# Optimization experiments

Hardware: AMD Instinct MI355X
Metric: run time of the kernel (lower is better)

The kernel has to match this reference:

```python
import jax, jax.numpy as jnp
import numpy as np
import math

B_, M_, T_, E_ = 4, 4, 128, 512
S_ = M_ * T_
H_ = 2048
NE, NS, TOPK, NHEAD = 8, 2, 2, 4
P_, GRUH, AK, AV = 128, 128, 64, 64


def _ln(x, s, b, eps=1e-5):
    mu = x.mean(-1, keepdims=True)
    var = x.var(-1, keepdims=True)
    return (x - mu) / jnp.sqrt(var + eps) * s + b


def _gru(x, Wih, bih, Whh, bhh):
    # x: [N, T, D] -> [N, T, GRUH]; torch nn.GRU cell equations
    Hh = Whh.shape[1]
    def step(h, xt):
        gi = xt @ Wih.T + bih
        gh = h @ Whh.T + bhh
        ir, iz, inn = jnp.split(gi, 3, axis=-1)
        hr, hz, hn = jnp.split(gh, 3, axis=-1)
        r = jax.nn.sigmoid(ir + hr)
        z = jax.nn.sigmoid(iz + hz)
        n = jnp.tanh(inn + r * hn)
        h = (1.0 - z) * n + z * h
        return h, h
    h0 = jnp.zeros((x.shape[0], Hh), x.dtype)
    _, hs = jax.lax.scan(step, h0, jnp.swapaxes(x, 0, 1))
    return jnp.swapaxes(hs, 0, 1)


def _router_logits(x4, rU, rR, rS, Wtp, btp, Wq, bq, Wk, bk, Wv, bv,
                   gWih, gbih, gWhh, gbhh, mW1, mb1, mW2, mb2):
    B, M, T, E = x4.shape
    proc = jax.nn.relu(x4 @ Wtp + btp)                  # [B,M,T,P]
    q = proc @ Wq + bq                                   # [B,M,T,AK]
    Rp = jnp.transpose(rR, (0, 3, 1, 2))                 # [B,T,M,M]
    Sp = jnp.transpose(rS, (0, 3, 1, 2))
    others = np.array([[j for j in range(M) if j != m] for m in range(M)])  # [M,M-1]
    mi = np.arange(M)[:, None]
    feat = jnp.stack([Rp[:, :, mi, others], Sp[:, :, mi, others]], axis=-1)  # [B,T,M,M-1,2]
    keys = feat @ Wk + bk                                # [B,T,M,M-1,AK]
    vals = feat @ Wv + bv                                # [B,T,M,M-1,AV]
    sc = jnp.einsum('bmtk,btmok->bmto', q, keys) / math.sqrt(AK)
    ctx = jnp.einsum('bmto,btmov->bmtv', jax.nn.softmax(sc, -1), vals)  # [B,M,T,AV]
    gin = jnp.concatenate([rU[..., None], ctx], -1).reshape(B * M, T, 1 + AV)
    hs = _gru(gin, gWih, gbih, gWhh, gbhh).reshape(B, M, T, GRUH)
    comb = jnp.concatenate([proc, hs], -1)               # [B,M,T,P+GRUH]
    return jax.nn.relu(comb @ mW1 + mb1) @ mW2 + mb2     # [B,M,T,NE]


def _forward(x, rU, rR, rS, M, T, Wtp, btp, Wq, bq, Wk, bk, Wv, bv,
             gWih, gbih, gWhh, gbhh, mW1, mb1, mW2, mb2,
             sWq, sbq, sWk, sbk, sWv, sbv, sWo, sbo, sln1s, sln1b,
             sW1, sb1, sW2, sb2, sln2s, sln2b, fW1, fb1, fW2, fb2):
    B, S, E = x.shape
    x4 = x.reshape(B, M, T, E)
    logits = _router_logits(x4, rU, rR, rS, Wtp, btp, Wq, bq, Wk, bk, Wv, bv,
                            gWih, gbih, gWhh, gbhh, mW1, mb1, mW2, mb2)
    NT = B * S
    lf = logits.reshape(NT, NE)
    probs = jax.nn.softmax(lf, -1)
    vals, idx = jax.lax.top_k(lf, TOPK)
    tw = jax.nn.softmax(vals, -1)                        # renormalized top-k weights
    tok = x.reshape(NT, E)
    out = jnp.zeros((NT, E), x.dtype)
    hd = E // NHEAD
    for e in range(NE):
        w = jnp.sum(jnp.where(idx == e, tw, 0.0), -1)    # [NT] per-token weight for expert e
        if e < NS:
            # synergy expert: self-attention restricted to tokens routed here.
            # Sort routed tokens to the front (fixed capacity NT) and mask keys.
            valid = w > 0
            order = jnp.argsort(jnp.where(valid, 0, 1), stable=True)
            xg, vg = tok[order], valid[order]
            qh = (xg @ sWq[e] + sbq[e]).reshape(NT, NHEAD, hd)
            kh = (xg @ sWk[e] + sbk[e]).reshape(NT, NHEAD, hd)
            vh = (xg @ sWv[e] + sbv[e]).reshape(NT, NHEAD, hd)
            sc = jnp.einsum('nhd,mhd->hnm', qh, kh) / math.sqrt(hd)
            sc = jnp.where(vg[None, None, :], sc, -1e9)
            ao = jnp.einsum('hnm,mhd->nhd', jax.nn.softmax(sc, -1), vh).reshape(NT, E)
            ao = ao @ sWo[e] + sbo[e]
            h1 = _ln(xg + ao, sln1s[e], sln1b[e])
            ff = jax.nn.relu(h1 @ sW1[e] + sb1[e]) @ sW2[e] + sb2[e]
            y = _ln(h1 + ff, sln2s[e], sln2b[e])
            out = out.at[order].add(y * w[order][:, None])
        else:
            # FFN expert is pointwise -> dense compute weighted by w (w==0 elsewhere)
            f = e - NS
            y = jax.nn.relu(tok @ fW1[f] + fb1[f]) @ fW2[f] + fb2[f]
            out = out + y * w[:, None]
    return (out.reshape(B, S, E), probs.reshape(B, M, T, NE),
            idx.reshape(B, M, T, TOPK))


def setup_inputs() -> dict:
    key = jax.random.key(0)
    ks = iter(jax.random.split(key, 64))
    def rn(shape, s=0.02):
        return jax.random.normal(next(ks), shape, dtype=jnp.float32) * s
    Cm = (P_ + GRUH) // 2
    return {
        'x': jax.random.normal(next(ks), (B_, S_, E_), dtype=jnp.float32),
        'rU': jax.random.uniform(next(ks), (B_, M_, T_), dtype=jnp.float32),
        'rR': jax.random.uniform(next(ks), (B_, M_, M_, T_), dtype=jnp.float32),
        'rS': jax.random.uniform(next(ks), (B_, M_, M_, T_), dtype=jnp.float32),
        'M': M_, 'T': T_,
        'Wtp': rn((E_, P_)), 'btp': jnp.zeros((P_,)),
        'Wq': rn((P_, AK)), 'bq': jnp.zeros((AK,)),
        'Wk': rn((2, AK)), 'bk': jnp.zeros((AK,)),
        'Wv': rn((2, AV)), 'bv': jnp.zeros((AV,)),
        'gWih': rn((3 * GRUH, 1 + AV)), 'gbih': jnp.zeros((3 * GRUH,)),
        'gWhh': rn((3 * GRUH, GRUH)), 'gbhh': jnp.zeros((3 * GRUH,)),
        'mW1': rn((P_ + GRUH, Cm)), 'mb1': jnp.zeros((Cm,)),
        'mW2': rn((Cm, NE)), 'mb2': jnp.zeros((NE,)),
        'sWq': rn((NS, E_, E_)), 'sbq': jnp.zeros((NS, E_)),
        'sWk': rn((NS, E_, E_)), 'sbk': jnp.zeros((NS, E_)),
        'sWv': rn((NS, E_, E_)), 'sbv': jnp.zeros((NS, E_)),
        'sWo': rn((NS, E_, E_)), 'sbo': jnp.zeros((NS, E_)),
        'sln1s': jnp.ones((NS, E_)), 'sln1b': jnp.zeros((NS, E_)),
        'sW1': rn((NS, E_, H_)), 'sb1': jnp.zeros((NS, H_)),
        'sW2': rn((NS, H_, E_)), 'sb2': jnp.zeros((NS, E_)),
        'sln2s': jnp.ones((NS, E_)), 'sln2b': jnp.zeros((NS, E_)),
        'fW1': rn((NE - NS, E_, H_)), 'fb1': jnp.zeros((NE - NS, H_)),
        'fW2': rn((NE - NS, H_, E_)), 'fb2': jnp.zeros((NE - NS, E_)),
    }


def reference(x, rU, rR, rS, M, T, Wtp, btp, Wq, bq, Wk, bk, Wv, bv,
              gWih, gbih, gWhh, gbhh, mW1, mb1, mW2, mb2,
              sWq, sbq, sWk, sbk, sWv, sbv, sWo, sbo, sln1s, sln1b,
              sW1, sb1, sW2, sb2, sln2s, sln2b, fW1, fb1, fW2, fb2):
    return _forward(x, rU, rR, rS, M, T, Wtp, btp, Wq, bq, Wk, bk, Wv, bv,
                    gWih, gbih, gWhh, gbhh, mW1, mb1, mW2, mb2,
                    sWq, sbq, sWk, sbk, sWv, sbv, sWo, sbo, sln1s, sln1b,
                    sW1, sb1, sW2, sb2, sln2s, sln2b, fW1, fb1, fW2, fb2)
```

## Files before the change

### kernel.cpp

```cpp
#include <hip/hip_runtime.h>
#include <math.h>

#define Bc 4
#define Mc 4
#define Tc 128
#define Ec 512
#define Hc 2048
#define NEc 8
#define NSc 2
#define NHEADc 4
#define Pc 128
#define GRUHc 128
#define AKc 64
#define AVc 64
#define NTc 2048
#define HDc 128

typedef __bf16 bfv8 __attribute__((ext_vector_type(8)));
typedef float f32x4 __attribute__((ext_vector_type(4)));

__global__ __launch_bounds__(256)
void zero_k(float* __restrict__ out, int* __restrict__ cnt,
            const float* __restrict__ gWih, float* __restrict__ gWihT)
{
    int i = blockIdx.x * 256 + threadIdx.x;
    float4* o4 = (float4*)out;
    if (i < (NTc * Ec) / 4) o4[i] = make_float4(0.f, 0.f, 0.f, 0.f);
    if (i < NEc) cnt[i] = 0;
    int j = i - (NTc * Ec) / 4;
    if (j >= 0 && j < 65 * 384) {
        int d = j / 384, g = j % 384;
        gWihT[j] = gWih[(size_t)g * 65 + d];
    }
}

__global__ __launch_bounds__(256)
void zspan_k(float* __restrict__ p, int n4)
{
    int i = blockIdx.x * 256 + threadIdx.x;
    if (i < n4) ((float4*)p)[i] = make_float4(0.f, 0.f, 0.f, 0.f);
}

struct CJob { const float* src; __bf16* dst; };
struct CJobs8 { CJob j[8]; };

__global__ __launch_bounds__(256)
void convT_k(CJobs8 jobs, int K, int N)
{
    CJob J = jobs.j[blockIdx.z];
    __shared__ float t[32][33];
    int bx = blockIdx.x * 32;
    int by = blockIdx.y * 32;
    int tx = threadIdx.x & 31, ty = threadIdx.x >> 5;
#pragma unroll
    for (int i = 0; i < 4; ++i) {
        int k = by + ty + i * 8, n = bx + tx;
        t[ty + i * 8][tx] = (k < K && n < N) ? J.src[(size_t)k * N + n] : 0.f;
    }
    __syncthreads();
#pragma unroll
    for (int i = 0; i < 4; ++i) {
        int n = bx + ty + i * 8, k = by + tx;
        if (n < N && k < K) J.dst[(size_t)n * K + k] = (__bf16)t[tx][ty + i * 8];
    }
}

__global__ __launch_bounds__(256)
void gemm_k(const float* __restrict__ A, int lda,
            const float* __restrict__ B, int ldb,
            const float* __restrict__ bias,
            float* __restrict__ C, int ldc,
            int M, int N, int K, int relu)
{
    int tm = blockIdx.x * 64, tn = blockIdx.y * 64;
    if (tm >= M || tn >= N) return;
    __shared__ float As[16][68];
    __shared__ float Bs[16][68];
    int tid = threadIdx.x;
    int tx = tid & 15, ty = tid >> 4;
    float acc[4][4] = {};
    int arow = tid >> 2;
    int ak0  = (tid & 3) * 4;
    int bk   = tid >> 4;
    int bc0  = (tid & 15) * 4;
    int grA = tm + arow;
    const float* Arow = (grA < M) ? (A + (size_t)grA * lda) : nullptr;

    for (int k0 = 0; k0 < K; k0 += 16) {
#pragma unroll
        for (int u = 0; u < 4; ++u) {
            int k = k0 + ak0 + u;
            As[ak0 + u][arow] = (Arow && k < K) ? Arow[k] : 0.f;
        }
        int kb = k0 + bk;
#pragma unroll
        for (int u = 0; u < 4; ++u) {
            int n2 = tn + bc0 + u;
            Bs[bk][bc0 + u] = (kb < K && n2 < N) ? B[(size_t)kb * ldb + n2] : 0.f;
        }
        __syncthreads();
#pragma unroll
        for (int kk = 0; kk < 16; ++kk) {
            float a0 = As[kk][ty * 4 + 0], a1 = As[kk][ty * 4 + 1];
            float a2 = As[kk][ty * 4 + 2], a3 = As[kk][ty * 4 + 3];
            float b0 = Bs[kk][tx * 4 + 0], b1 = Bs[kk][tx * 4 + 1];
            float b2 = Bs[kk][tx * 4 + 2], b3 = Bs[kk][tx * 4 + 3];
            acc[0][0] += a0 * b0; acc[0][1] += a0 * b1; acc[0][2] += a0 * b2; acc[0][3] += a0 * b3;
            acc[1][0] += a1 * b0; acc[1][1] += a1 * b1; acc[1][2] += a1 * b2; acc[1][3] += a1 * b3;
            acc[2][0] += a2 * b0; acc[2][1] += a2 * b1; acc[2][2] += a2 * b2; acc[2][3] += a2 * b3;
            acc[3][0] += a3 * b0; acc[3][1] += a3 * b1; acc[3][2] += a3 * b2; acc[3][3] += a3 * b3;
        }
        __syncthreads();
    }
#pragma unroll
    for (int i = 0; i < 4; ++i) {
        int gr = tm + ty * 4 + i;
        if (gr >= M) continue;
#pragma unroll
        for (int j = 0; j < 4; ++j) {
            int gc = tn + tx * 4 + j;
            if (gc >= N) continue;
            float v = acc[i][j] + (bias ? bias[gc] : 0.f);
            if (relu) v = fmaxf(v, 0.f);
            C[(size_t)gr * ldc + gc] = v;
        }
    }
}

struct GJob {
    const void* A;
    const void* B;
    const float* bias;
    void* C;
    const int* Mptr;
    const int* gatherA;
    float* scatterOut;
    const int* scatterList;
    const float* wvec;
    int ldc;
    int flags;
};
struct GJobs6 { GJob j[6]; };

#define LDA_S 40
template<int AMODE>
__global__ __launch_bounds__(256)
void gemm_batch_k(GJobs6 jobs, int lda, int ldb, int N, int K,
                  int nTilesY, int kIters)
{
    GJob J = jobs.j[blockIdx.z];
    int M = *J.Mptr;
    int by = blockIdx.y;
    int ny = by % nTilesY, ko = by / nTilesY;
    int tm = blockIdx.x * 128, tn = ny * 128;
    if (tm >= M || tn >= N) return;
    int KT = K / 32;
    int kt0 = ko * kIters;
    int ktE = kt0 + kIters; if (ktE > KT) ktE = KT;
    if (kt0 >= KT) return;

    __shared__ __bf16 As[128 * LDA_S];
    __shared__ __bf16 Bs[128 * LDA_S];
    int tid = threadIdx.x, lane = tid & 63, wvi = tid >> 6;
    int wm = (wvi & 1) * 64, wn = (wvi >> 1) * 64;
    f32x4 acc[4][4] = {};

    int ar = tid >> 1, ah = (tid & 1) * 16;
    const float*  Apf = nullptr;
    const __bf16* Apb = nullptr;
    if (tm + ar < M) {
        int g = J.gatherA ? J.gatherA[tm + ar] : (tm + ar);
        if (AMODE == 0) Apf = (const float*)J.A + (size_t)g * lda;
        else            Apb = (const __bf16*)J.A + (size_t)g * lda;
    }
    const __bf16* Bp = ((tn + ar) < N) ? ((const __bf16*)J.B + (size_t)(tn + ar) * ldb)
                                       : nullptr;

    float fa[16];
    bfv8 ra0, ra1, rb0, rb1;

    auto LOADA = [&](int k0) {
        int kb = k0 + ah;
        if (AMODE == 0) {
            if (Apf) {
                const float4* p = (const float4*)(Apf + kb);
                float4 x0 = p[0], x1 = p[1], x2 = p[2], x3 = p[3];
                fa[0]=x0.x; fa[1]=x0.y; fa[2]=x0.z; fa[3]=x0.w;
                fa[4]=x1.x; fa[5]=x1.y; fa[6]=x1.z; fa[7]=x1.w;
                fa[8]=x2.x; fa[9]=x2.y; fa[10]=x2.z; fa[11]=x2.w;
                fa[12]=x3.x; fa[13]=x3.y; fa[14]=x3.z; fa[15]=x3.w;
            } else {
#pragma unroll
                for (int i = 0; i < 16; ++i) fa[i] = 0.f;
            }
        } else {
            if (Apb) {
                ra0 = *(const bfv8*)(Apb + kb);
                ra1 = *(const bfv8*)(Apb + kb + 8);
            } else {
#pragma unroll
                for (int i = 0; i < 8; ++i) { ra0[i] = (__bf16)0.f; ra1[i] = (__bf16)0.f; }
            }
        }
    };
    auto LOADB = [&](int k0) {
        int kb = k0 + ah;
        if (Bp) {
            rb0 = *(const bfv8*)(Bp + kb);
            rb1 = *(const bfv8*)(Bp + kb + 8);
        } else {
#pragma unroll
            for (int i = 0; i < 8; ++i) { rb0[i] = (__bf16)0.f; rb1[i] = (__bf16)0.f; }
        }
    };

    LOADA(kt0 * 32);
    LOADB(kt0 * 32);

    for (int kt = kt0; kt < ktE; ++kt) {
        __syncthreads();
        if (AMODE == 0) {
            bfv8 p0, p1;
#pragma unroll
            for (int i = 0; i < 8; ++i) { p0[i] = (__bf16)fa[i]; p1[i] = (__bf16)fa[8 + i]; }
            *(bfv8*)(As + ar * LDA_S + ah) = p0;
            *(bfv8*)(As + ar * LDA_S + ah + 8) = p1;
        } else {
            *(bfv8*)(As + ar * LDA_S + ah) = ra0;
            *(bfv8*)(As + ar * LDA_S + ah + 8) = ra1;
        }
        *(bfv8*)(Bs + ar * LDA_S + ah) = rb0;
        *(bfv8*)(Bs + ar * LDA_S + ah + 8) = rb1;
        __syncthreads();
        if (kt + 1 < ktE) {
            LOADA((kt + 1) * 32);
            LOADB((kt + 1) * 32);
        }
        {
            int fr = lane & 15, quad = lane >> 4;
            bfv8 af[4], bfr[4];
            const __bf16* Ab = As + quad * 8 + fr * LDA_S;
            const __bf16* Bb2 = Bs + quad * 8 + fr * LDA_S;
#pragma unroll
            for (int t2 = 0; t2 < 4; ++t2) {
                af[t2]  = *(const bfv8*)(Ab + (wm + t2 * 16) * LDA_S);
                bfr[t2] = *(const bfv8*)(Bb2 + (wn + t2 * 16) * LDA_S);
            }
#pragma unroll
            for (int i = 0; i < 4; ++i)
#pragma unroll
                for (int j = 0; j < 4; ++j)
                    acc[i][j] = __builtin_amdgcn_mfma_f32_16x16x32_bf16(af[i], bfr[j], acc[i][j], 0, 0, 0);
        }
    }

    int col = lane & 15, rq = (lane >> 4) * 4;
    int relu = J.flags & 1, storeT = J.flags & 2, storeBf = J.flags & 4;
    int accum = J.flags & 8;
    int addBias = (J.bias != nullptr) && (ko == 0);
#pragma unroll
    for (int ti = 0; ti < 4; ++ti) {
#pragma unroll
        for (int tj = 0; tj < 4; ++tj) {
#pragma unroll
            for (int r = 0; r < 4; ++r) {
                int gm = tm + wm + ti * 16 + rq + r;
                int gn = tn + wn + tj * 16 + col;
                if (gm < M && gn < N) {
                    float v = acc[ti][tj][r] + (addBias ? J.bias[gn] : 0.f);
                    if (relu) v = fmaxf(v, 0.f);
                    if (J.scatterOut) {
                        int g = J.scatterList[gm];
                        atomicAdd(&J.scatterOut[(size_t)g * Ec + gn], v * J.wvec[(size_t)g * NEc]);
                    } else if (accum) {
                        atomicAdd(&((float*)J.C)[(size_t)gm * J.ldc + gn], v);
                    } else if (storeT) {
                        ((float*)J.C)[(size_t)gn * J.ldc + gm] = v;
                    } else if (storeBf) {
                        ((__bf16*)J.C)[(size_t)gm * J.ldc + gn] = (__bf16)v;
                    } else {
                        ((float*)J.C)[(size_t)gm * J.ldc + gn] = v;
                    }
                }
            }
        }
    }
}

__global__ __launch_bounds__(256)
void flash_k(const float* __restrict__ QbB, const float* __restrict__ KbB,
             const float* __restrict__ VtB, float* __restrict__ AOB,
             const int* __restrict__ cntB)
{
    int e = blockIdx.z;
    const float* Qb = QbB + (size_t)e * NTc * Ec;
    const float* Kb = KbB + (size_t)e * NTc * Ec;
    const float* Vt = VtB + (size_t)e * NTc * Ec;
    float* AO = AOB + (size_t)e * NTc * Ec;
    int nv = cntB[e];
    int r0 = blockIdx.x * 64;
    if (r0 >= nv) return;
    int h = blockIdx.y;
    const int QS = 136, VS = 72;
    __shared__ __bf16 Ql[64 * 136];
    __shared__ __bf16 Kl[64 * 136];
    __shared__ __bf16 Vl[128 * 72];
    __shared__ __bf16 Pl[64 * 72];
    int tid = threadIdx.x, lane = tid & 63, wv = tid >> 6;
    int fr = lane & 15, quad = lane >> 4;

    {
        int qr = tid >> 2, c0 = (tid & 3) * 32;
        const float* src = Qb + (size_t)(r0 + qr) * Ec + h * HDc + c0;
        __bf16* dst = Ql + qr * QS + c0;
        bool ok = (r0 + qr) < nv;
#pragma unroll
        for (int u = 0; u < 8; ++u) {
            float4 v = ok ? ((const float4*)src)[u] : make_float4(0.f, 0.f, 0.f, 0.f);
            dst[u*4+0] = (__bf16)v.x; dst[u*4+1] = (__bf16)v.y;
            dst[u*4+2] = (__bf16)v.z; dst[u*4+3] = (__bf16)v.w;
        }
    }

    f32x4 accO[8];
#pragma unroll
    for (int j = 0; j < 8; ++j) accO[j] = (f32x4){0.f, 0.f, 0.f, 0.f};
    float mrow[4] = {-1e30f, -1e30f, -1e30f, -1e30f};
    float lrow[4] = {0.f, 0.f, 0.f, 0.f};
    const float invsq = 0.08838834764831845f;

    for (int j0 = 0; j0 < nv; j0 += 64) {
        __syncthreads();
        {
            int kr = tid >> 2, c0 = (tid & 3) * 32;
            const float* src = Kb + (size_t)(j0 + kr) * Ec + h * HDc + c0;
            __bf16* dst = Kl + kr * QS + c0;
            bool ok = (j0 + kr) < nv;
#pragma unroll
            for (int u = 0; u < 8; ++u) {
                float4 v = ok ? ((const float4*)src)[u] : make_float4(0.f, 0.f, 0.f, 0.f);
                dst[u*4+0] = (__bf16)v.x; dst[u*4+1] = (__bf16)v.y;
                dst[u*4+2] = (__bf16)v.z; dst[u*4+3] = (__bf16)v.w;
            }
        }
        {
            int dr = tid >> 1, c0 = (tid & 1) * 32;
            const float* src = Vt + (size_t)(h * HDc + dr) * NTc + j0 + c0;
            __bf16* dst = Vl + dr * VS + c0;
            int rem = nv - (j0 + c0);
            if (rem >= 32) {
#pragma unroll
                for (int u = 0; u < 8; ++u) {
                    float4 v = ((const float4*)src)[u];
                    dst[u*4+0] = (__bf16)v.x; dst[u*4+1] = (__bf16)v.y;
                    dst[u*4+2] = (__bf16)v.z; dst[u*4+3] = (__bf16)v.w;
                }
            } else {
                for (int u = 0; u < 32; ++u)
                    dst[u] = (u < rem) ? (__bf16)src[u] : (__bf16)0.f;
            }
        }
        __syncthreads();

        f32x4 sc[4] = {};
#pragma unroll
        for (int ks = 0; ks < 4; ++ks) {
            bfv8 aq = *(const bfv8*)(Ql + (wv * 16 + fr) * QS + ks * 32 + quad * 8);
#pragma unroll
            for (int tj = 0; tj < 4; ++tj) {
                bfv8 bk8 = *(const bfv8*)(Kl + (tj * 16 + fr) * QS + ks * 32 + quad * 8);
                sc[tj] = __builtin_amdgcn_mfma_f32_16x16x32_bf16(aq, bk8, sc[tj], 0, 0, 0);
            }
        }

        float alpha[4];
#pragma unroll
        for (int r = 0; r < 4; ++r) {
            float sv[4];
            float mx = -1e30f;
#pragma unroll
            for (int tj = 0; tj < 4; ++tj) {
                float s = sc[tj][r] * invsq;
                bool valid = (j0 + tj * 16 + fr) < nv;
                s = valid ? s : -1e30f;
                sv[tj] = s;
                mx = fmaxf(mx, s);
            }
#pragma unroll
            for (int off = 1; off < 16; off <<= 1)
                mx = fmaxf(mx, __shfl_xor(mx, off, 64));
            float mn = fmaxf(mrow[r], mx);
            alpha[r] = expf(mrow[r] - mn);
            float ps = 0.f;
#pragma unroll
            for (int tj = 0; tj < 4; ++tj) {
                bool valid = (j0 + tj * 16 + fr) < nv;
                float p = valid ? expf(sv[tj] - mn) : 0.f;
                Pl[(wv * 16 + quad * 4 + r) * VS + tj * 16 + fr] = (__bf16)p;
                ps += p;
            }
#pragma unroll
            for (int off = 1; off < 16; off <<= 1)
                ps += __shfl_xor(ps, off, 64);
            lrow[r] = lrow[r] * alpha[r] + ps;
            mrow[r] = mn;
        }
#pragma unroll
        for (int tj = 0; tj < 8; ++tj)
#pragma unroll
            for (int r = 0; r < 4; ++r)
                accO[tj][r] *= alpha[r];
#pragma unroll
        for (int ks = 0; ks < 2; ++ks) {
            bfv8 ap = *(const bfv8*)(Pl + (wv * 16 + fr) * VS + ks * 32 + quad * 8);
#pragma unroll
            for (int tj = 0; tj < 8; ++tj) {
                bfv8 bv8 = *(const bfv8*)(Vl + (tj * 16 + fr) * VS + ks * 32 + quad * 8);
                accO[tj] = __builtin_amdgcn_mfma_f32_16x16x32_bf16(ap, bv8, accO[tj], 0, 0, 0);
            }
        }
    }

#pragma unroll
    for (int r = 0; r < 4; ++r) {
        int row = r0 + wv * 16 + quad * 4 + r;
        if (row < nv) {
            float invl = 1.f / lrow[r];
#pragma unroll
            for (int tj = 0; tj < 8; ++tj)
                AO[(size_t)row * Ec + h * HDc + tj * 16 + fr] = accO[tj][r] * invl;
        }
    }
}

__global__ __launch_bounds__(256)
void router_ctx_k(const float* __restrict__ q4, const float* __restrict__ rR,
                  const float* __restrict__ rS,
                  const float* __restrict__ Wk, const float* __restrict__ bk,
                  const float* __restrict__ Wv, const float* __restrict__ bv,
                  float* __restrict__ ctx)
{
    int tid = threadIdx.x;
    int lane = tid & 63;
    int n = blockIdx.x * 4 + (tid >> 6);
    int m = (n >> 7) & 3, t = n & 127, b = n >> 9;
    float q = q4[(size_t)n * AKc + lane];
    float sc[3], rv[3], sv[3];
#pragma unroll
    for (int o = 0; o < 3; ++o) {
        int oth = o + (o >= m ? 1 : 0);
        float r = rR[(((size_t)(b * Mc + m)) * Mc + oth) * Tc + t];
        float s_ = rS[(((size_t)(b * Mc + m)) * Mc + oth) * Tc + t];
        rv[o] = r; sv[o] = s_;
        float key = r * Wk[lane] + s_ * Wk[64 + lane] + bk[lane];
        float p = q * key;
#pragma unroll
        for (int off = 32; off; off >>= 1) p += __shfl_xor(p, off, 64);
        sc[o] = p * 0.125f;
    }
    float mx = fmaxf(sc[0], fmaxf(sc[1], sc[2]));
    float e0 = expf(sc[0] - mx), e1 = expf(sc[1] - mx), e2 = expf(sc[2] - mx);
    float inv = 1.f / (e0 + e1 + e2);
    float p0 = e0 * inv, p1 = e1 * inv, p2 = e2 * inv;
    float v0 = rv[0] * Wv[lane] + sv[0] * Wv[64 + lane] + bv[lane];
    float v1 = rv[1] * Wv[lane] + sv[1] * Wv[64 + lane] + bv[lane];
    float v2 = rv[2] * Wv[lane] + sv[2] * Wv[64 + lane] + bv[lane];
    ctx[(size_t)n * AVc + lane] = p0 * v0 + p1 * v1 + p2 * v2;
}

__global__ __launch_bounds__(384)
void gi_k(const float* __restrict__ rU, const float* __restrict__ ctx,
          const float* __restrict__ WT, const float* __restrict__ gbih,
          float* __restrict__ gi)
{
    int nt = blockIdx.x;
    int g = threadIdx.x;
    __shared__ float cl[64];
    if (g < 64) cl[g] = ctx[(size_t)nt * AVc + g];
    __syncthreads();
    float a = gbih[g] + rU[nt] * WT[g];
#pragma unroll
    for (int d = 0; d < 64; ++d) a += cl[d] * WT[(size_t)(1 + d) * 384 + g];
    gi[(size_t)nt * 384 + g] = a;
}

__device__ __forceinline__ void wgbar()
{
    __builtin_amdgcn_sched_barrier(0);
    asm volatile("s_waitcnt lgkmcnt(0)" ::: "memory");
    __builtin_amdgcn_s_barrier();
    __builtin_amdgcn_sched_barrier(0);
}

__global__ __launch_bounds__(1024) __attribute__((amdgpu_waves_per_eu(4, 4)))
void gru_scan_k(const float* __restrict__ gi, const float* __restrict__ gWhh,
                const float* __restrict__ gbhh, float* __restrict__ hs)
{
    int seq = blockIdx.x, tid = threadIdx.x;
    int work = (tid < 768);
    int g = work ? (tid >> 1) : 0;
    int half = tid & 1;
    __shared__ float h[136];
    __shared__ float gh[384];
    const f32x4* wp = (const f32x4*)(gWhh + (size_t)g * 128 + half * 64);
    f32x4 w0 = wp[0],  w1 = wp[1],  w2 = wp[2],  w3 = wp[3];
    f32x4 w4 = wp[4],  w5 = wp[5],  w6 = wp[6],  w7 = wp[7];
    f32x4 w8 = wp[8],  w9 = wp[9],  wA = wp[10], wB = wp[11];
    f32x4 wC = wp[12], wD = wp[13], wE = wp[14], wF = wp[15];
    float bh = gbhh[g];

    float hreg = 0.f, c0 = 0.f, c1 = 0.f, c2 = 0.f;
    int hi = tid + ((tid >> 6) << 2);
    if (tid < 128) {
        h[hi] = 0.f;
        const float* gr = gi + (size_t)seq * 128 * 384;
        c0 = gr[tid]; c1 = gr[128 + tid]; c2 = gr[256 + tid];
    }
    wgbar();

    for (int t = 0; t < 128; ++t) {
        asm volatile("" : "+v"(w0), "+v"(w1), "+v"(w2), "+v"(w3),
                          "+v"(w4), "+v"(w5), "+v"(w6), "+v"(w7),
                          "+v"(w8), "+v"(w9), "+v"(wA), "+v"(wB),
                          "+v"(wC), "+v"(wD), "+v"(wE), "+v"(wF));
        float n0 = 0.f, n1 = 0.f, n2 = 0.f;
        if (tid < 128 && t + 1 < 128) {
            const float* gr = gi + ((size_t)seq * 128 + t + 1) * 384;
            n0 = gr[tid]; n1 = gr[128 + tid]; n2 = gr[256 + tid];
        }
        if (work) {
            float a0 = 0.f, a1 = 0.f, a2 = 0.f, a3 = 0.f;
            const float* hb = h + half * 68;
#define GRU_STEP4(W, B) { \
            f32x4 x = *(const f32x4*)&hb[B]; \
            a0 += x[0] * W[0]; a1 += x[1] * W[1]; a2 += x[2] * W[2]; a3 += x[3] * W[3]; }
            GRU_STEP4(w0, 0)   GRU_STEP4(w1, 4)   GRU_STEP4(w2, 8)   GRU_STEP4(w3, 12)
            GRU_STEP4(w4, 16)  GRU_STEP4(w5, 20)  GRU_STEP4(w6, 24)  GRU_STEP4(w7, 28)
            GRU_STEP4(w8, 32)  GRU_STEP4(w9, 36)  GRU_STEP4(wA, 40)  GRU_STEP4(wB, 44)
            GRU_STEP4(wC, 48)  GRU_STEP4(wD, 52)  GRU_STEP4(wE, 56)  GRU_STEP4(wF, 60)
#undef GRU_STEP4
            float s = (a0 + a1) + (a2 + a3);
            s += __shfl_xor(s, 1, 64);
            if (half == 0) gh[g] = s + bh;
        }
        wgbar();
        if (tid < 128) {
            float ghr = gh[tid], ghz = gh[128 + tid], ghn = gh[256 + tid];
            float r  = 1.f / (1.f + expf(-(c0 + ghr)));
            float z  = 1.f / (1.f + expf(-(c1 + ghz)));
            float nn = tanhf(c2 + r * ghn);
            float hn = (1.f - z) * nn + z * hreg;
            hs[((size_t)seq * 128 + t) * 128 + tid] = hn;
            h[hi] = hn;
            hreg = hn;
            c0 = n0; c1 = n1; c2 = n2;
        }
        wgbar();
    }
}

__global__ __launch_bounds__(128)
void mlp_route_k(const float* __restrict__ proc, const float* __restrict__ hs,
                 const float* __restrict__ mW1, const float* __restrict__ mb1,
                 const float* __restrict__ mW2, const float* __restrict__ mb2,
                 float* __restrict__ probsOut, float* __restrict__ idxOut,
                 float* __restrict__ w)
{
    int n = blockIdx.x, tid = threadIdx.x;
    __shared__ float comb[256], tmp[128], lg[8];
    comb[tid] = proc[(size_t)n * 128 + tid];
    comb[128 + tid] = hs[(size_t)n * 128 + tid];
    __syncthreads();
    float a = mb1[tid];
#pragma unroll 8
    for (int d = 0; d < 256; ++d) a += comb[d] * mW1[(size_t)d * 128 + tid];
    tmp[tid] = fmaxf(a, 0.f);
    __syncthreads();
    if (tid < 8) {
        float l = mb2[tid];
        for (int d = 0; d < 128; ++d) l += tmp[d] * mW2[(size_t)d * 8 + tid];
        lg[tid] = l;
    }
    __syncthreads();
    if (tid == 0) {
        float mx = lg[0];
        for (int e = 1; e < 8; ++e) mx = fmaxf(mx, lg[e]);
        float p[8], s = 0.f;
        for (int e = 0; e < 8; ++e) { p[e] = expf(lg[e] - mx); s += p[e]; }
        float inv = 1.f / s;
        for (int e = 0; e < 8; ++e) probsOut[(size_t)n * 8 + e] = p[e] * inv;
        int a0 = 0; float v0 = lg[0];
        for (int e = 1; e < 8; ++e) if (lg[e] > v0) { v0 = lg[e]; a0 = e; }
        int a1 = -1; float v1 = -1e30f;
        for (int e = 0; e < 8; ++e) if (e != a0 && lg[e] > v1) { v1 = lg[e]; a1 = e; }
        float e1 = expf(v1 - v0);
        float t0 = 1.f / (1.f + e1), t1 = e1 / (1.f + e1);
        idxOut[(size_t)n * 2 + 0] = (float)a0;
        idxOut[(size_t)n * 2 + 1] = (float)a1;
        for (int e = 0; e < 8; ++e) w[(size_t)n * 8 + e] = 0.f;
        w[(size_t)n * 8 + a0] = t0;
        w[(size_t)n * 8 + a1] = t1;
    }
}

__global__ __launch_bounds__(256)
void compact_k(const float* __restrict__ w, int* __restrict__ cnt,
               int* __restrict__ list)
{
    int n = blockIdx.x * 256 + threadIdx.x;
    if (n >= NTc) return;
    for (int e = 0; e < NEc; ++e)
        if (w[(size_t)n * 8 + e] > 0.f) {
            int p = atomicAdd(&cnt[e], 1);
            list[e * NTc + p] = n;
        }
}

__global__ __launch_bounds__(256)
void ln1_k(const float* __restrict__ x, const int* __restrict__ listB,
           const float* __restrict__ addB, const float* __restrict__ sB,
           const float* __restrict__ bB, float* __restrict__ outB,
           const int* __restrict__ cntB)
{
    int e = blockIdx.y;
    int i = blockIdx.x;
    if (i >= cntB[e]) return;
    const int* list = listB + e * NTc;
    const float* add = addB + (size_t)e * NTc * Ec;
    const float* s = sB + e * Ec;
    const float* b = bB + e * Ec;
    float* outRows = outB + (size_t)e * NTc * Ec;
    int tid = threadIdx.x;
    int g = list[i];
    float v0 = x[(size_t)g * Ec + tid] + add[(size_t)i * Ec + tid];
    float v1 = x[(size_t)g * Ec + 256 + tid] + add[(size_t)i * Ec + 256 + tid];
    __shared__ float red[256];
    __shared__ float bc;
    red[tid] = v0 + v1; __syncthreads();
    for (int st = 128; st > 0; st >>= 1) { if (tid < st) red[tid] += red[tid + st]; __syncthreads(); }
    if (tid == 0) bc = red[0] * (1.f / 512.f);
    __syncthreads();
    float mu = bc;
    float d0 = v0 - mu, d1 = v1 - mu;
    __syncthreads();
    red[tid] = d0 * d0 + d1 * d1; __syncthreads();
    for (int st = 128; st > 0; st >>= 1) { if (tid < st) red[tid] += red[tid + st]; __syncthreads(); }
    if (tid == 0) bc = rsqrtf(red[0] * (1.f / 512.f) + 1e-5f);
    __syncthreads();
    float inv = bc;
    outRows[(size_t)i * Ec + tid] = d0 * inv * s[tid] + b[tid];
    outRows[(size_t)i * Ec + 256 + tid] = d1 * inv * s[256 + tid] + b[256 + tid];
}

__global__ __launch_bounds__(256)
void ln2_scatter_k(const float* __restrict__ H1B, const float* __restrict__ YB,
                   const float* __restrict__ sB, const float* __restrict__ bB,
                   float* __restrict__ out, const int* __restrict__ listB,
                   const int* __restrict__ cntB, const float* __restrict__ wB)
{
    int e = blockIdx.y;
    int i = blockIdx.x;
    if (i >= cntB[e]) return;
    const int* list = listB + e * NTc;
    const float* H1 = H1B + (size_t)e * NTc * Ec;
    const float* Y = YB + (size_t)e * NTc * Ec;
    const float* s = sB + e * Ec;
    const float* b = bB + e * Ec;
    const float* wvec = wB + e;
    int tid = threadIdx.x;
    int g = list[i];
    float v0 = H1[(size_t)i * Ec + tid] + Y[(size_t)i * Ec + tid];
    float v1 = H1[(size_t)i * Ec + 256 + tid] + Y[(size_t)i * Ec + 256 + tid];
    __shared__ float red[256];
    __shared__ float bc;
    red[tid] = v0 + v1; __syncthreads();
    for (int st = 128; st > 0; st >>= 1) { if (tid < st) red[tid] += red[tid + st]; __syncthreads(); }
    if (tid == 0) bc = red[0] * (1.f / 512.f);
    __syncthreads();
    float mu = bc;
    float d0 = v0 - mu, d1 = v1 - mu;
    __syncthreads();
    red[tid] = d0 * d0 + d1 * d1; __syncthreads();
    for (int st = 128; st > 0; st >>= 1) { if (tid < st) red[tid] += red[tid + st]; __syncthreads(); }
    if (tid == 0) bc = rsqrtf(red[0] * (1.f / 512.f) + 1e-5f);
    __syncthreads();
    float inv = bc;
    float wv = wvec[(size_t)g * 8];
    atomicAdd(&out[(size_t)g * Ec + tid], (d0 * inv * s[tid] + b[tid]) * wv);
    atomicAdd(&out[(size_t)g * Ec + 256 + tid], (d1 * inv * s[256 + tid] + b[256 + tid]) * wv);
}

extern "C" void kernel_launch(void* const* d_in, const int* in_sizes, int n_in,
                              void* d_out, int out_size, void* d_ws, size_t ws_size,
                              hipStream_t stream)
{
    const float* x    = (const float*)d_in[0];
    const float* rU   = (const float*)d_in[1];
    const float* rR   = (const float*)d_in[2];
    const float* rS   = (const float*)d_in[3];
    const float* Wtp  = (const float*)d_in[6];
    const float* btp  = (const float*)d_in[7];
    const float* Wq   = (const float*)d_in[8];
    const float* bq   = (const float*)d_in[9];
    const float* Wk   = (const float*)d_in[10];
    const float* bk   = (const float*)d_in[11];
    const float* Wv   = (const float*)d_in[12];
    const float* bv   = (const float*)d_in[13];
    const float* gWih = (const float*)d_in[14];
    const float* gbih = (const float*)d_in[15];
    const float* gWhh = (const float*)d_in[16];
    const float* gbhh = (const float*)d_in[17];
    const float* mW1  = (const float*)d_in[18];
    const float* mb1  = (const float*)d_in[19];
    const float* mW2  = (const float*)d_in[20];
    const float* mb2  = (const float*)d_in[21];
    const float* sWq  = (const float*)d_in[22];
    const float* sbq  = (const float*)d_in[23];
    const float* sWk  = (const float*)d_in[24];
    const float* sbk  = (const float*)d_in[25];
    const float* sWv  = (const float*)d_in[26];
    const float* sbv  = (const float*)d_in[27];
    const float* sWo  = (const float*)d_in[28];
    const float* sbo  = (const float*)d_in[29];
    const float* sln1s = (const float*)d_in[30];
    const float* sln1b = (const float*)d_in[31];
    const float* sW1  = (const float*)d_in[32];
    const float* sb1  = (const float*)d_in[33];
    const float* sW2  = (const float*)d_in[34];
    const float* sb2  = (const float*)d_in[35];
    const float* sln2s = (const float*)d_in[36];
    const float* sln2b = (const float*)d_in[37];
    const float* fW1  = (const float*)d_in[38];
    const float* fb1  = (const float*)d_in[39];
    const float* fW2  = (const float*)d_in[40];
    const float* fb2  = (const float*)d_in[41];

    float* out      = (float*)d_out;
    float* probsOut = out + (size_t)NTc * Ec;
    float* idxOut   = probsOut + (size_t)NTc * NEc;

    int*   cnt  = (int*)d_ws;
    int*   list = cnt + 64;
    float* w    = (float*)d_ws + 64 + NEc * NTc;
    __bf16* WB = (__bf16*)(w + NTc * NEc);
    auto QKVO_T = [&](int e, int i) { return WB + ((size_t)(e * 4 + i)) * 262144; };
    __bf16* sW1T = WB + 8 * 262144;
    __bf16* sW2T = sW1T + 2 * 1048576;
    __bf16* fW1T = sW2T + 2 * 1048576;
    __bf16* fW2T = fW1T + 3 * 1048576;
    float* act = (float*)(fW2T + 3 * 1048576);
    float* QbB = act;
    float* KbB = act + 2 * 1048576;
    float* VtB = act + 4 * 1048576;
    float* AOB = act + 6 * 1048576;
    float* H1B = act + 8 * 1048576;
    float* PRJB = QbB;
    float* YbB  = KbB;
    __bf16* FF1syn = (__bf16*)VtB;
    __bf16* FF1ffn = (__bf16*)act;
    __bf16* fW1T2 = FF1ffn + (size_t)3 * NTc * Hc;
    __bf16* fW2T2 = fW1T2 + 3 * 1048576;
    float* proc = act;
    float* q4   = act + 262144;
    float* ctx  = act + 393216;
    float* gi   = act + 524288;
    float* hs   = act + 1310720;
    float* gWihT = act + 1572864;

    zero_k<<<1122, 256, 0, stream>>>(out, cnt, gWih, gWihT);

    gemm_k<<<dim3(32, 2), 256, 0, stream>>>(x, Ec, Wtp, Pc, btp, proc, Pc, NTc, Pc, Ec, 1);
    gemm_k<<<dim3(32, 1), 256, 0, stream>>>(proc, Pc, Wq, AKc, bq, q4, AKc, NTc, AKc, Pc, 0);
    router_ctx_k<<<512, 256, 0, stream>>>(q4, rR, rS, Wk, bk, Wv, bv, ctx);
    gi_k<<<2048, 384, 0, stream>>>(rU, ctx, gWihT, gbih, gi);
    gru_scan_k<<<16, 1024, 0, stream>>>(gi, gWhh, gbhh, hs);
    mlp_route_k<<<2048, 128, 0, stream>>>(proc, hs, mW1, mb1, mW2, mb2,
                                          probsOut, idxOut, w);
    compact_k<<<8, 256, 0, stream>>>(w, cnt, list);

    GJob JZ = {};

    {
        CJobs8 cq = {};
        for (int e = 0; e < 2; ++e) {
            cq.j[e * 4 + 0] = { sWq + (size_t)e * Ec * Ec, QKVO_T(e, 0) };
            cq.j[e * 4 + 1] = { sWk + (size_t)e * Ec * Ec, QKVO_T(e, 1) };
            cq.j[e * 4 + 2] = { sWv + (size_t)e * Ec * Ec, QKVO_T(e, 2) };
            cq.j[e * 4 + 3] = { sWo + (size_t)e * Ec * Ec, QKVO_T(e, 3) };
        }
        convT_k<<<dim3(16, 16, 8), 256, 0, stream>>>(cq, Ec, Ec);
        CJobs8 c1 = {};
        c1.j[0] = { sW1, sW1T };
        c1.j[1] = { sW1 + (size_t)Ec * Hc, sW1T + 1048576 };
        convT_k<<<dim3(64, 16, 2), 256, 0, stream>>>(c1, Ec, Hc);
        CJobs8 c2 = {};
        c2.j[0] = { sW2, sW2T };
        c2.j[1] = { sW2 + (size_t)Hc * Ec, sW2T + 1048576 };
        convT_k<<<dim3(16, 64, 2), 256, 0, stream>>>(c2, Hc, Ec);
    }

    {
        GJobs6 js = {};
        for (int e = 0; e < 2; ++e) {
            GJob jq = JZ;
            jq.A = x; jq.Mptr = cnt + e; jq.gatherA = list + e * NTc;
            jq.B = QKVO_T(e, 0); jq.bias = sbq + e * Ec;
            jq.C = QbB + (size_t)e * NTc * Ec; jq.ldc = Ec; jq.flags = 0;
            GJob jk = jq; jk.B = QKVO_T(e, 1); jk.bias = sbk + e * Ec;
            jk.C = KbB + (size_t)e * NTc * Ec;
            GJob jv = jq; jv.B = QKVO_T(e, 2); jv.bias = sbv + e * Ec;
            jv.C = VtB + (size_t)e * NTc * Ec; jv.ldc = NTc; jv.flags = 2;
            js.j[e * 3 + 0] = jq; js.j[e * 3 + 1] = jk; js.j[e * 3 + 2] = jv;
        }
        gemm_batch_k<0><<<dim3(16, 4, 6), 256, 0, stream>>>(js, Ec, Ec, Ec, Ec, 4, 16);
    }

    flash_k<<<dim3(32, 4, 2), 256, 0, stream>>>(QbB, KbB, VtB, AOB, cnt);

    zspan_k<<<4096, 256, 0, stream>>>(act, 1048576);

    {
        GJobs6 js = {};
        for (int e = 0; e < 2; ++e) {
            GJob jo = JZ;
            jo.A = AOB + (size_t)e * NTc * Ec; jo.Mptr = cnt + e;
            jo.B = QKVO_T(e, 3); jo.bias = sbo + e * Ec;
            jo.C = PRJB + (size_t)e * NTc * Ec; jo.ldc = Ec; jo.flags = 8;
            js.j[e] = jo;
        }
        gemm_batch_k<0><<<dim3(16, 16, 2), 256, 0, stream>>>(js, Ec, Ec, Ec, Ec, 4, 4);
    }

    ln1_k<<<dim3(2048, 2), 256, 0, stream>>>(x, list, PRJB, sln1s, sln1b, H1B, cnt);

    {
        GJobs6 js = {};
        for (int e = 0; e < 2; ++e) {
            GJob j1 = JZ;
            j1.A = H1B + (size_t)e * NTc * Ec; j1.Mptr = cnt + e;
            j1.B = sW1T + (size_t)e * 1048576; j1.bias = sb1 + (size_t)e * Hc;
            j1.C = FF1syn + (size_t)e * NTc * Hc; j1.ldc = Hc; j1.flags = 1 | 4;
            js.j[e] = j1;
        }
        gemm_batch_k<0><<<dim3(16, 16, 2), 256, 0, stream>>>(js, Ec, Ec, Hc, Ec, 16, 16);
    }

    {
        GJobs6 js = {};
        for (int e = 0; e < 2; ++e) {
            GJob j2 = JZ;
            j2.A = FF1syn + (size_t)e * NTc * Hc; j2.Mptr = cnt + e;
            j2.B = sW2T + (size_t)e * 1048576; j2.bias = sb2 + (size_t)e * Ec;
            j2.C = YbB + (size_t)e * NTc * Ec; j2.ldc = Ec; j2.flags = 8;
            js.j[e] = j2;
        }
        gemm_batch_k<1><<<dim3(16, 16, 2), 256, 0, stream>>>(js, Hc, Hc, Ec, Hc, 4, 16);
    }

    ln2_scatter_k<<<dim3(2048, 2), 256, 0, stream>>>(H1B, YbB, sln2s, sln2b,
                                                     out, list, cnt, w);

    {
        CJobs8 a = {};
        for (int u = 0; u < 6; ++u)
            a.j[u] = { fW1 + (size_t)u * Ec * Hc,
                       (u < 3 ? fW1T + (size_t)u * 1048576
                              : fW1T2 + (size_t)(u - 3) * 1048576) };
        convT_k<<<dim3(64, 16, 6), 256, 0, stream>>>(a, Ec, Hc);
        CJobs8 b = {};
        for (int u = 0; u < 6; ++u)
            b.j[u] = { fW2 + (size_t)u * Hc * Ec,
                       (u < 3 ? fW2T + (size_t)u * 1048576
                              : fW2T2 + (size_t)(u - 3) * 1048576) };
        convT_k<<<dim3(16, 64, 6), 256, 0, stream>>>(b, Hc, Ec);
    }

    for (int rnd = 0; rnd < 2; ++rnd) {
        int f0 = rnd * 3;
        __bf16* W1 = rnd == 0 ? fW1T : fW1T2;
        __bf16* W2 = rnd == 0 ? fW2T : fW2T2;
        {
            GJobs6 js = {};
            for (int u = 0; u < 3; ++u) {
                int f = f0 + u, e = f + NSc;
                GJob j1 = JZ;
                j1.A = x; j1.Mptr = cnt + e; j1.gatherA = list + e * NTc;
                j1.B = W1 + (size_t)u * 1048576; j1.bias = fb1 + (size_t)f * Hc;
                j1.C = FF1ffn + (size_t)u * NTc * Hc; j1.ldc = Hc; j1.flags = 1 | 4;
                js.j[u] = j1;
            }
            gemm_batch_k<0><<<dim3(16, 16, 3), 256, 0, stream>>>(js, Ec, Ec, Hc, Ec, 16, 16);
        }
        {
            GJobs6 js = {};
            for (int u = 0; u < 3; ++u) {
                int f = f0 + u, e = f + NSc;
                GJob j2 = JZ;
                j2.A = FF1ffn + (size_t)u * NTc * Hc; j2.Mptr = cnt + e;
                j2.B = W2 + (size_t)u * 1048576; j2.bias = fb2 + (size_t)f * Ec;
                j2.scatterOut = out; j2.scatterList = list + e * NTc;
                j2.wvec = w + e; j2.ldc = Ec;
                js.j[u] = j2;
            }
            gemm_batch_k<1><<<dim3(16, 16, 3), 256, 0, stream>>>(js, Hc, Hc, Ec, Hc, 4, 16);
        }
    }
}
```

Baseline: 918.0 us.

## Replace router GEMMs with row-blocked kernels and drop split-K atomics

Replaces the generic 64x64 tiled fp32 GEMM used for the router projection and query with dedicated kernels. Each block stages four token rows in shared memory and streams weight columns, giving 512 blocks instead of 32 or 64 so the GPU is better filled. Removes the split-K atomic accumulation (flag 8) from the output-projection and FFN2 batched GEMMs by covering the full K in each block, which also drops the zeroing kernel that cleared their accumulators. Each FFN2 block now walks the whole K range serially, which reduces parallelism there.

Result: faster. 878.2 us (-4.3%).

```diff
diff --git a/kernel.cpp b/kernel.cpp
--- a/kernel.cpp
+++ b/kernel.cpp
@@ -34,13 +34,6 @@
     }
 }
 
-__global__ __launch_bounds__(256)
-void zspan_k(float* __restrict__ p, int n4)
-{
-    int i = blockIdx.x * 256 + threadIdx.x;
-    if (i < n4) ((float4*)p)[i] = make_float4(0.f, 0.f, 0.f, 0.f);
-}
-
 struct CJob { const float* src; __bf16* dst; };
 struct CJobs8 { CJob j[8]; };
 
@@ -66,65 +59,45 @@
 }
 
 __global__ __launch_bounds__(256)
-void gemm_k(const float* __restrict__ A, int lda,
-            const float* __restrict__ B, int ldb,
-            const float* __restrict__ bias,
-            float* __restrict__ C, int ldc,
-            int M, int N, int K, int relu)
-{
-    int tm = blockIdx.x * 64, tn = blockIdx.y * 64;
-    if (tm >= M || tn >= N) return;
-    __shared__ float As[16][68];
-    __shared__ float Bs[16][68];
-    int tid = threadIdx.x;
-    int tx = tid & 15, ty = tid >> 4;
-    float acc[4][4] = {};
-    int arow = tid >> 2;
-    int ak0  = (tid & 3) * 4;
-    int bk   = tid >> 4;
-    int bc0  = (tid & 15) * 4;
-    int grA = tm + arow;
-    const float* Arow = (grA < M) ? (A + (size_t)grA * lda) : nullptr;
-
-    for (int k0 = 0; k0 < K; k0 += 16) {
-#pragma unroll
-        for (int u = 0; u < 4; ++u) {
-            int k = k0 + ak0 + u;
-            As[ak0 + u][arow] = (Arow && k < K) ? Arow[k] : 0.f;
-        }
-        int kb = k0 + bk;
-#pragma unroll
-        for (int u = 0; u < 4; ++u) {
-            int n2 = tn + bc0 + u;
-            Bs[bk][bc0 + u] = (kb < K && n2 < N) ? B[(size_t)kb * ldb + n2] : 0.f;
-        }
-        __syncthreads();
-#pragma unroll
-        for (int kk = 0; kk < 16; ++kk) {
-            float a0 = As[kk][ty * 4 + 0], a1 = As[kk][ty * 4 + 1];
-            float a2 = As[kk][ty * 4 + 2], a3 = As[kk][ty * 4 + 3];
-            float b0 = Bs[kk][tx * 4 + 0], b1 = Bs[kk][tx * 4 + 1];
-            float b2 = Bs[kk][tx * 4 + 2], b3 = Bs[kk][tx * 4 + 3];
-            acc[0][0] += a0 * b0; acc[0][1] += a0 * b1; acc[0][2] += a0 * b2; acc[0][3] += a0 * b3;
-            acc[1][0] += a1 * b0; acc[1][1] += a1 * b1; acc[1][2] += a1 * b2; acc[1][3] += a1 * b3;
-            acc[2][0] += a2 * b0; acc[2][1] += a2 * b1; acc[2][2] += a2 * b2; acc[2][3] += a2 * b3;
-            acc[3][0] += a3 * b0; acc[3][1] += a3 * b1; acc[3][2] += a3 * b2; acc[3][3] += a3 * b3;
-        }
-        __syncthreads();
-    }
-#pragma unroll
-    for (int i = 0; i < 4; ++i) {
-        int gr = tm + ty * 4 + i;
-        if (gr >= M) continue;
-#pragma unroll
-        for (int j = 0; j < 4; ++j) {
-            int gc = tn + tx * 4 + j;
-            if (gc >= N) continue;
-            float v = acc[i][j] + (bias ? bias[gc] : 0.f);
-            if (relu) v = fmaxf(v, 0.f);
-            C[(size_t)gr * ldc + gc] = v;
-        }
-    }
+void proc_k(const float* __restrict__ x, const float* __restrict__ Wtp,
+            const float* __restrict__ btp, float* __restrict__ proc)
+{
+    int b = blockIdx.x, tid = threadIdx.x;
+    int j = tid & 127, half = tid >> 7;
+    __shared__ float xs[4 * Ec];
+    const float4* src = (const float4*)(x + (size_t)b * 4 * Ec);
+    ((float4*)xs)[tid] = src[tid];
+    ((float4*)xs)[256 + tid] = src[256 + tid];
+    __syncthreads();
+    const float* x0 = xs + (half * 2) * Ec;
+    const float* x1 = xs + (half * 2 + 1) * Ec;
+    float a0 = 0.f, a1 = 0.f;
+#pragma unroll 8
+    for (int k = 0; k < Ec; ++k) {
+        float wv = Wtp[(size_t)k * Pc + j];
+        a0 += x0[k] * wv;
+        a1 += x1[k] * wv;
+    }
+    int t0 = b * 4 + half * 2;
+    proc[(size_t)t0 * Pc + j]       = fmaxf(a0 + btp[j], 0.f);
+    proc[(size_t)(t0 + 1) * Pc + j] = fmaxf(a1 + btp[j], 0.f);
+}
+
+__global__ __launch_bounds__(256)
+void q4_k(const float* __restrict__ proc, const float* __restrict__ Wq,
+          const float* __restrict__ bq, float* __restrict__ q4)
+{
+    int b = blockIdx.x, tid = threadIdx.x;
+    int j = tid & 63, tk = tid >> 6;
+    __shared__ float pr[4 * Pc];
+    const float2* src = (const float2*)(proc + (size_t)b * 4 * Pc);
+    ((float2*)pr)[tid] = src[tid];
+    __syncthreads();
+    const float* p = pr + tk * Pc;
+    float a = 0.f;
+#pragma unroll 8
+    for (int k = 0; k < Pc; ++k) a += p[k] * Wq[(size_t)k * AKc + j];
+    q4[(size_t)(b * 4 + tk) * AKc + j] = a + bq[j];
 }
 
 struct GJob {
@@ -769,8 +742,8 @@
 
     zero_k<<<1122, 256, 0, stream>>>(out, cnt, gWih, gWihT);
 
-    gemm_k<<<dim3(32, 2), 256, 0, stream>>>(x, Ec, Wtp, Pc, btp, proc, Pc, NTc, Pc, Ec, 1);
-    gemm_k<<<dim3(32, 1), 256, 0, stream>>>(proc, Pc, Wq, AKc, bq, q4, AKc, NTc, AKc, Pc, 0);
+    proc_k<<<512, 256, 0, stream>>>(x, Wtp, btp, proc);
+    q4_k<<<512, 256, 0, stream>>>(proc, Wq, bq, q4);
     router_ctx_k<<<512, 256, 0, stream>>>(q4, rR, rS, Wk, bk, Wv, bv, ctx);
     gi_k<<<2048, 384, 0, stream>>>(rU, ctx, gWihT, gbih, gi);
     gru_scan_k<<<16, 1024, 0, stream>>>(gi, gWhh, gbhh, hs);
@@ -817,18 +790,16 @@
 
     flash_k<<<dim3(32, 4, 2), 256, 0, stream>>>(QbB, KbB, VtB, AOB, cnt);
 
-    zspan_k<<<4096, 256, 0, stream>>>(act, 1048576);
-
     {
         GJobs6 js = {};
         for (int e = 0; e < 2; ++e) {
             GJob jo = JZ;
             jo.A = AOB + (size_t)e * NTc * Ec; jo.Mptr = cnt + e;
             jo.B = QKVO_T(e, 3); jo.bias = sbo + e * Ec;
-            jo.C = PRJB + (size_t)e * NTc * Ec; jo.ldc = Ec; jo.flags = 8;
+            jo.C = PRJB + (size_t)e * NTc * Ec; jo.ldc = Ec;
             js.j[e] = jo;
         }
-        gemm_batch_k<0><<<dim3(16, 16, 2), 256, 0, stream>>>(js, Ec, Ec, Ec, Ec, 4, 4);
+        gemm_batch_k<0><<<dim3(16, 4, 2), 256, 0, stream>>>(js, Ec, Ec, Ec, Ec, 4, 16);
     }
 
     ln1_k<<<dim3(2048, 2), 256, 0, stream>>>(x, list, PRJB, sln1s, sln1b, H1B, cnt);
@@ -851,10 +822,10 @@
             GJob j2 = JZ;
             j2.A = FF1syn + (size_t)e * NTc * Hc; j2.Mptr = cnt + e;
             j2.B = sW2T + (size_t)e * 1048576; j2.bias = sb2 + (size_t)e * Ec;
-            j2.C = YbB + (size_t)e * NTc * Ec; j2.ldc = Ec; j2.flags = 8;
+            j2.C = YbB + (size_t)e * NTc * Ec; j2.ldc = Ec;
             js.j[e] = j2;
         }
-        gemm_batch_k<1><<<dim3(16, 16, 2), 256, 0, stream>>>(js, Hc, Hc, Ec, Hc, 4, 16);
+        gemm_batch_k<1><<<dim3(16, 4, 2), 256, 0, stream>>>(js, Hc, Hc, Ec, Hc, 4, 64);
     }
 
     ln2_scatter_k<<<dim3(2048, 2), 256, 0, stream>>>(H1B, YbB, sln2s, sln2b,
```
